# Optimization experiments

Measured on AMD Instinct MI355X. Metric: run time of the kernel, lower is better.

## Reference

```python
import jax, jax.numpy as jnp
import numpy as np
from jax import lax

BIN_NUM = 48
CPG = BIN_NUM * 3            # 144 hidden channels
NOUT = BIN_NUM + 1           # 49 symbols
K = 5                        # masked conv kernel size
H, W = 256, 512
TABLE_TOTAL = 65536.0        # EntropyTable total frequency
SCALE = 2.0 / (BIN_NUM - 1.0)


def _causal_mask(include_center: bool) -> jnp.ndarray:
    # Raster-scan causal 5x5 mask: all rows above center, left of center in
    # center row; center tap only for 'hidden' (mask-B) layers.
    m = np.zeros((K, K), np.float32)
    c = K // 2
    m[:c, :] = 1.0
    m[c, :c] = 1.0
    if include_center:
        m[c, c] = 1.0
    return jnp.asarray(m)[None, None]  # broadcast over (O, I, kh, kw)


def _mconv(x, w, b, mask):
    # x: (N, C, H, W); w: (O, I, K, K)
    y = lax.conv_general_dilated(
        x, w * mask, window_strides=(1, 1), padding='SAME',
        dimension_numbers=('NCHW', 'OIHW', 'NCHW'))
    return y + b[None, :, None, None]


def setup_inputs() -> dict:
    key = jax.random.key(0)
    ks = jax.random.split(key, 8)
    # quantized code indices in [0, BIN_NUM)
    data = jax.random.randint(ks[0], (1, 1, H, W), 0, BIN_NUM).astype(jnp.float32)
    s0 = 1.0 / np.sqrt(1 * K * K)
    sr = 1.0 / np.sqrt(CPG * K * K)
    w0 = jax.random.normal(ks[1], (CPG, 1, K, K), jnp.float32) * s0
    b0 = jnp.zeros((CPG,), jnp.float32)
    # 5 residual blocks x 2 convs = 10 hidden masked convs, stacked
    wres = jax.random.normal(ks[2], (10, CPG, CPG, K, K), jnp.float32) * sr
    bres = jnp.zeros((10, CPG), jnp.float32)
    wl = jax.random.normal(ks[3], (NOUT, CPG, K, K), jnp.float32) * sr
    bl = jnp.zeros((NOUT,), jnp.float32)
    return {"data": data, "w0": w0, "b0": b0, "wres": wres, "bres": bres,
            "wl": wl, "bl": bl}


def reference(data, w0, b0, wres, bres, wl, bl):
    mask_a = _causal_mask(False)   # first layer excludes center pixel
    mask_b = _causal_mask(True)    # hidden layers include center pixel

    # Scale(-1, 2/(bin_num-1)): map codes [0, bin_num-1] -> [-1, 1]
    x = data * SCALE - 1.0
    x = jax.nn.relu(_mconv(x, w0, b0, mask_a))
    # 5 residual blocks: y = relu(conv(relu(conv(x)))) + x
    for i in range(5):
        h1 = jax.nn.relu(_mconv(x, wres[2 * i], bres[2 * i], mask_b))
        h2 = jax.nn.relu(_mconv(h1, wres[2 * i + 1], bres[2 * i + 1], mask_b))
        x = x + h2
    logits = _mconv(x, wl, bl, mask_b)          # (1, 49, H, W)

    # EntropyTable: per-pixel softmax -> cumulative frequency table (total 65536)
    probs = jax.nn.softmax(logits, axis=1)
    cdf = jnp.cumsum(probs, axis=1) * TABLE_TOTAL
    zeros = jnp.zeros((cdf.shape[0], 1) + cdf.shape[2:], cdf.dtype)
    vec = jnp.concatenate([zeros, cdf], axis=1)  # (1, 50, H, W)
    return vec
```

## Files before the change

### kernel.cpp

```cpp
#include <hip/hip_runtime.h>

#define HH 256
#define WW 512
#define CPG 144
#define NKG 18
#define WP 516
#define HPADR 258
#define XB_E ((size_t)NKG * HPADR * WP * 8)
#define NCH 59
#define KREAL 1872
#define SCALE_F (2.0f / 47.0f)

typedef __attribute__((ext_vector_type(8))) short short8;
typedef __attribute__((ext_vector_type(4))) float floatx4;

__device__ __forceinline__ unsigned short f2bf(float f) {
    unsigned u = __builtin_bit_cast(unsigned, f);
    u += 0x7FFFu + ((u >> 16) & 1u);
    return (unsigned short)(u >> 16);
}
__device__ __forceinline__ float bf2f(unsigned short h) {
    unsigned u = ((unsigned)h) << 16;
    return __builtin_bit_cast(float, u);
}
__device__ __forceinline__ void async16(const void* g, void* l) {
    __builtin_amdgcn_global_load_lds(
        (const __attribute__((address_space(1))) unsigned int*)g,
        (__attribute__((address_space(3))) unsigned int*)l, 16, 0, 0);
}
__device__ __forceinline__ void tap_decode(int t, int& kh, int& kw) {
    kh = t < 5 ? 0 : (t < 10 ? 1 : 2);
    kw = t - (t < 5 ? 0 : (t < 10 ? 5 : 10));
}

__global__ void k_zero(float* __restrict__ p, size_t n4) {
    size_t i = (size_t)blockIdx.x * blockDim.x + threadIdx.x;
    size_t stride = (size_t)gridDim.x * blockDim.x;
    float4 z = make_float4(0.f, 0.f, 0.f, 0.f);
    for (; i < n4; i += stride) ((float4*)p)[i] = z;
}

__global__ void k_pack_hidden(const float* __restrict__ wres, unsigned short* __restrict__ wpk) {
    const int total = 10 * NCH * CPG * 32;
    int i = blockIdx.x * blockDim.x + threadIdx.x;
    int stride = gridDim.x * blockDim.x;
    for (; i < total; i += stride) {
        int kk = i & 31;
        int q  = i >> 5;
        int co = q % CPG;
        int c  = (q / CPG) % NCH;
        int l  = q / (CPG * NCH);
        int K = c * 32 + kk;
        float v = 0.f;
        if (K < KREAL) {
            int t = K / CPG, ci = K - t * CPG;
            int kh, kw; tap_decode(t, kh, kw);
            v = wres[(((size_t)(l * CPG + co) * CPG + ci) * 5 + kh) * 5 + kw];
        }
        wpk[i] = f2bf(v);
    }
}
__global__ void k_pack_final(const float* __restrict__ wl, unsigned short* __restrict__ wpkF) {
    const int total = NCH * 64 * 32;
    int i = blockIdx.x * blockDim.x + threadIdx.x;
    if (i >= total) return;
    int kk = i & 31;
    int co = (i >> 5) & 63;
    int c  = i >> 11;
    int K = c * 32 + kk;
    float v = 0.f;
    if (K < KREAL && co < 49) {
        int t = K / CPG, ci = K - t * CPG;
        int kh, kw; tap_decode(t, kh, kw);
        v = wl[(((size_t)co * CPG + ci) * 5 + kh) * 5 + kw];
    }
    wpkF[i] = f2bf(v);
}
__global__ void k_pack_small(const float* __restrict__ w0, const float* __restrict__ bl,
                             float* __restrict__ w0p, float* __restrict__ blp) {
    int i = blockIdx.x * blockDim.x + threadIdx.x;
    if (i < 12 * CPG) {
        int co = i % CPG, t = i / CPG;
        int kh, kw; tap_decode(t, kh, kw);
        w0p[i] = w0[co * 25 + kh * 5 + kw];
    } else if (i < 12 * CPG + 64) {
        int k = i - 12 * CPG;
        blp[k] = k < 49 ? bl[k] : 0.f;
    }
}

__global__ __launch_bounds__(384) void k_layer0(
    const float* __restrict__ data, const float* __restrict__ w0p,
    const float* __restrict__ b0, unsigned short* __restrict__ Xb) {
    const int lane = threadIdx.x;
    const int x = blockIdx.x * 64 + lane;
    const int y = blockIdx.y;

    float xv[12];
#pragma unroll
    for (int t = 0; t < 12; t++) {
        int kh, kw; tap_decode(t, kh, kw);
        int yy = y + kh - 2, xx = x + kw - 2;
        xv[t] = (yy >= 0 && xx >= 0 && xx < WW) ? data[yy * WW + xx] * SCALE_F - 1.0f : 0.f;
    }
#pragma unroll
    for (int kgi = 0; kgi < 3; kgi++) {
        int kg = threadIdx.y * 3 + kgi;
        float a8[8];
#pragma unroll
        for (int j = 0; j < 8; j++) a8[j] = 0.f;
#pragma unroll
        for (int t = 0; t < 12; t++)
#pragma unroll
            for (int j = 0; j < 8; j++)
                a8[j] = fmaf(w0p[t * CPG + kg * 8 + j], xv[t], a8[j]);
        short8 o;
#pragma unroll
        for (int j = 0; j < 8; j++)
            o[j] = (short)f2bf(fmaxf(a8[j] + b0[kg * 8 + j], 0.f));
        *(short8*)&Xb[((size_t)(kg * HPADR + y + 2) * WP + (x + 2)) * 8] = o;
    }
}

template<bool RES>
__global__ __launch_bounds__(768, 3) void k_conv(
    const unsigned short* __restrict__ in,
    const unsigned short* __restrict__ wq,
    const float* __restrict__ bias,
    const unsigned short* __restrict__ res,
    unsigned short* __restrict__ out) {
    __shared__ __align__(16) unsigned short As[NKG][4][132][8];
    __shared__ unsigned toff[NCH][4];
    const int tid  = threadIdx.x;
    const int lane = tid & 63;
    const int wid  = tid >> 6;
    const int ng   = wid % 3;
    const int r    = (wid / 3) & 1;
    const int ph   = wid / 6;
    const int lr = lane & 15;
    const int lg = lane >> 4;

    const int fid = blockIdx.x + (int)gridDim.x * blockIdx.y;
    const int swz = (fid & 7) * 64 + (fid >> 3);
    const int x0 = (swz & 3) * 128;
    const int y0 = (swz >> 2) * 2;

    floatx4 acc[4][3];
#pragma unroll
    for (int m = 0; m < 4; m++)
#pragma unroll
        for (int n = 0; n < 3; n++) acc[m][n] = (floatx4)0.f;

    for (int i = wid; i < 144; i += 12) {
        int half = i & 1;
        int rr   = (i >> 1) & 3;
        int kg   = i >> 3;
        async16(in + ((size_t)(kg * HPADR + y0 + rr) * WP + x0 + half * 64 + lane) * 8,
                &As[kg][rr][half * 64][0]);
    }
    if (tid < 288) {
        int kg = tid >> 4;
        int rr = (tid >> 2) & 3;
        int pxl = 128 + (tid & 3);
        *(short8*)&As[kg][rr][pxl][0] =
            *(const short8*)(in + ((size_t)(kg * HPADR + y0 + rr) * WP + x0 + pxl) * 8);
    }
    if (tid < NCH * 4) {
        int c = tid >> 2, l2 = tid & 3;
        int g = c * 4 + l2;
        if (g > 233) g = 233;
        int t = (g * 57) >> 10;
        int kgp = g - t * 18;
        int kh, kw; tap_decode(t, kh, kw);
        toff[c][l2] = (unsigned)(((kgp * 4 + kh) * 132 + kw) * 16);
    }
    asm volatile("s_waitcnt vmcnt(0) lgkmcnt(0)" ::: "memory");
    __builtin_amdgcn_s_barrier();
    __builtin_amdgcn_sched_barrier(0);

    const char* abase = (const char*)&As[0][r][ph * 64 + lr][0];
    auto LDA = [&](int c, short8 (&a)[4]) {
        const unsigned short* ap = (const unsigned short*)(abase + toff[c][lg]);
#pragma unroll
        for (int m = 0; m < 4; ++m) a[m] = *(const short8*)(ap + m * 16 * 8);
    };
    auto LDB = [&](int c, short8 (&b)[3]) {
        const unsigned short* bp = wq + (size_t)c * 4608 + (ng * 48 + lr) * 32 + lg * 8;
#pragma unroll
        for (int n = 0; n < 3; ++n) b[n] = *(const short8*)(bp + n * 512);
    };
    auto CMP = [&](const short8 (&a)[4], const short8 (&b)[3]) {
#pragma unroll
        for (int m = 0; m < 4; ++m)
#pragma unroll
            for (int n = 0; n < 3; ++n)
                acc[m][n] = __builtin_amdgcn_mfma_f32_16x16x32_bf16(a[m], b[n], acc[m][n], 0, 0, 0);
    };

    short8 a0[4], b0_[3], a1[4], b1_[3];
    LDB(0, b0_); LDA(0, a0);
#pragma unroll 1
    for (int c = 0; c < 58; c += 2) {
        LDB(c + 1, b1_); LDA(c + 1, a1);
        CMP(a0, b0_);
        LDB(c + 2, b0_); LDA(c + 2, a0);
        CMP(a1, b1_);
    }
    CMP(a0, b0_);

#pragma unroll
    for (int n = 0; n < 3; ++n) {
        int co = ng * 48 + n * 16 + lr;
        float bv = bias[co];
        const size_t pb = ((size_t)((co >> 3) * HPADR + y0 + 2 + r) * WP + (x0 + 2)) * 8 + (co & 7);
#pragma unroll
        for (int m = 0; m < 4; ++m)
#pragma unroll
            for (int rr = 0; rr < 4; ++rr) {
                int px = ph * 64 + m * 16 + lg * 4 + rr;
                size_t o = pb + (size_t)px * 8;
                float v = fmaxf(acc[m][n][rr] + bv, 0.f);
                if (RES) v += bf2f(res[o]);
                out[o] = f2bf(v);
            }
    }
}

__global__ __launch_bounds__(256, 2) void k_logits(
    const unsigned short* __restrict__ in,
    const unsigned short* __restrict__ wq,
    const float* __restrict__ blp,
    float* __restrict__ logits) {
    const int lane = threadIdx.x & 63;
    const int wid  = threadIdx.x >> 6;
    const int lr = lane & 15;
    const int lg = lane >> 4;
    const int tt = blockIdx.x * 4 + wid;
    const int y  = tt >> 2;
    const int x0 = (tt & 3) * 128;

    floatx4 acc[8][4];
#pragma unroll
    for (int m = 0; m < 8; m++)
#pragma unroll
        for (int n = 0; n < 4; n++) acc[m][n] = (floatx4)0.f;

#pragma unroll 1
    for (int c = 0; c < NCH; ++c) {
        int g = c * 4 + lg;
        if (g > 233) g = 233;
        int t = (g * 57) >> 10;
        int kgp = g - t * 18;
        int kh, kw; tap_decode(t, kh, kw);
        const unsigned short* ap =
            in + ((size_t)(kgp * HPADR + y + kh) * WP + (x0 + kw + lr)) * 8;
        const unsigned short* bp =
            wq + ((size_t)c * 64 + lr) * 32 + lg * 8;
        short8 a[8], b[4];
#pragma unroll
        for (int m = 0; m < 8; ++m) a[m] = *(const short8*)(ap + m * 128);
#pragma unroll
        for (int n = 0; n < 4; ++n) b[n] = *(const short8*)(bp + n * 512);
#pragma unroll
        for (int m = 0; m < 8; ++m)
#pragma unroll
            for (int n = 0; n < 4; ++n)
                acc[m][n] = __builtin_amdgcn_mfma_f32_16x16x32_bf16(
                    a[m], b[n], acc[m][n], 0, 0, 0);
    }

#pragma unroll
    for (int n = 0; n < 4; ++n) {
        int co = n * 16 + lr;
        float bv = blp[co];
#pragma unroll
        for (int m = 0; m < 8; ++m)
#pragma unroll
            for (int rr = 0; rr < 4; ++rr) {
                int px = m * 16 + lg * 4 + rr;
                logits[((size_t)y * WW + x0 + px) * 64 + co] = acc[m][n][rr] + bv;
            }
    }
}

__global__ __launch_bounds__(256) void k_softmax(
    const float* __restrict__ lg, float* __restrict__ out) {
    const int px = blockIdx.x * 256 + threadIdx.x;
    const int y = blockIdx.y;
    const size_t p = (size_t)y * WW + px;
    const float* l = lg + p * 64;
    float v[49];
    float m = -1e30f;
#pragma unroll
    for (int k = 0; k < 49; k++) { v[k] = l[k]; m = fmaxf(m, v[k]); }
    float s = 0.f;
#pragma unroll
    for (int k = 0; k < 49; k++) {
        v[k] = exp2f((v[k] - m) * 1.44269504088896f);
        s += v[k];
    }
    const float inv = 65536.0f / s;
    out[p] = 0.f;
    float run = 0.f;
#pragma unroll
    for (int k = 0; k < 49; k++) {
        run += v[k];
        out[(size_t)(k + 1) * (HH * WW) + p] = run * inv;
    }
}

extern "C" void kernel_launch(void* const* d_in, const int* in_sizes, int n_in,
                              void* d_out, int out_size, void* d_ws, size_t ws_size,
                              hipStream_t stream) {
    (void)in_sizes; (void)n_in; (void)out_size; (void)ws_size;
    const float* data = (const float*)d_in[0];
    const float* w0   = (const float*)d_in[1];
    const float* b0   = (const float*)d_in[2];
    const float* wres = (const float*)d_in[3];
    const float* bres = (const float*)d_in[4];
    const float* wl   = (const float*)d_in[5];
    const float* bl   = (const float*)d_in[6];
    float* out = (float*)d_out;

    char* ws = (char*)d_ws;
    unsigned short* Xb   = (unsigned short*)ws;
    unsigned short* Hb   = Xb + XB_E;
    unsigned short* wpk  = Hb + XB_E;
    unsigned short* wpkF = wpk + (size_t)10 * NCH * CPG * 32;
    float* blp  = (float*)(wpkF + (size_t)NCH * 64 * 32);
    float* w0p  = blp + 64;
    float* logits = w0p + 1728;

    k_zero<<<2048, 256, 0, stream>>>((float*)ws, (2 * XB_E * 2) / 16);

    k_pack_hidden<<<2048, 256, 0, stream>>>(wres, wpk);
    k_pack_final<<<(NCH * 64 * 32 + 255) / 256, 256, 0, stream>>>(wl, wpkF);
    k_pack_small<<<7, 256, 0, stream>>>(w0, bl, w0p, blp);

    k_layer0<<<dim3(8, 256), dim3(64, 6), 0, stream>>>(data, w0p, b0, Xb);

    const size_t LSTRIDE = (size_t)NCH * CPG * 32;
    for (int i = 0; i < 5; i++) {
        k_conv<false><<<dim3(4, 128), 768, 0, stream>>>(
            Xb, wpk + (size_t)(2 * i) * LSTRIDE, bres + (2 * i) * CPG, Xb, Hb);
        k_conv<true><<<dim3(4, 128), 768, 0, stream>>>(
            Hb, wpk + (size_t)(2 * i + 1) * LSTRIDE, bres + (2 * i + 1) * CPG, Xb, Xb);
    }

    k_logits<<<256, 256, 0, stream>>>(Xb, wpkF, blp, logits);
    k_softmax<<<dim3(2, 256), 256, 0, stream>>>(logits, out);
}
```

Baseline: 977.1 us.

## Stage logits conv input in LDS and add MFMA priority hints

Rewrites the final logits convolution to stage a 2-row by 128-pixel input halo tile in shared memory and read shifted taps from LDS, instead of each wave gathering taps from global memory. The block grows to 8 waves split across output-channel halves, rows and pixel halves, with a swizzled block order and a double-buffered load/compute loop. It also wraps the MFMA bursts in both conv kernels with sched_barrier and s_setprio so compute issues at raised priority. The cost being targeted is repeated global reads of overlapping taps and unhidden load latency, in exchange for LDS footprint and lower occupancy.

```diff
diff --git a/kernel.cpp b/kernel.cpp
--- a/kernel.cpp
+++ b/kernel.cpp
@@ -190,11 +190,15 @@
         for (int n = 0; n < 3; ++n) b[n] = *(const short8*)(bp + n * 512);
     };
     auto CMP = [&](const short8 (&a)[4], const short8 (&b)[3]) {
+        __builtin_amdgcn_sched_barrier(0);
+        __builtin_amdgcn_s_setprio(1);
 #pragma unroll
         for (int m = 0; m < 4; ++m)
 #pragma unroll
             for (int n = 0; n < 3; ++n)
                 acc[m][n] = __builtin_amdgcn_mfma_f32_16x16x32_bf16(a[m], b[n], acc[m][n], 0, 0, 0);
+        __builtin_amdgcn_s_setprio(0);
+        __builtin_amdgcn_sched_barrier(0);
     };
 
     short8 a0[4], b0_[3], a1[4], b1_[3];
@@ -226,59 +230,104 @@
     }
 }
 
-__global__ __launch_bounds__(256, 2) void k_logits(
+__global__ __launch_bounds__(512, 2) void k_logits(
     const unsigned short* __restrict__ in,
     const unsigned short* __restrict__ wq,
     const float* __restrict__ blp,
     float* __restrict__ logits) {
-    const int lane = threadIdx.x & 63;
-    const int wid  = threadIdx.x >> 6;
+    __shared__ __align__(16) unsigned short As[NKG][4][132][8];
+    __shared__ unsigned toff[NCH][4];
+    const int tid  = threadIdx.x;
+    const int lane = tid & 63;
+    const int wid  = tid >> 6;
+    const int ng   = wid & 1;
+    const int r    = (wid >> 1) & 1;
+    const int ph   = wid >> 2;
     const int lr = lane & 15;
     const int lg = lane >> 4;
-    const int tt = blockIdx.x * 4 + wid;
-    const int y  = tt >> 2;
-    const int x0 = (tt & 3) * 128;
-
-    floatx4 acc[8][4];
-#pragma unroll
-    for (int m = 0; m < 8; m++)
-#pragma unroll
-        for (int n = 0; n < 4; n++) acc[m][n] = (floatx4)0.f;
-
-#pragma unroll 1
-    for (int c = 0; c < NCH; ++c) {
-        int g = c * 4 + lg;
+
+    const int fid = blockIdx.x + (int)gridDim.x * blockIdx.y;
+    const int swz = (fid & 7) * 64 + (fid >> 3);
+    const int x0 = (swz & 3) * 128;
+    const int y0 = (swz >> 2) * 2;
+
+    floatx4 acc[4][2];
+#pragma unroll
+    for (int m = 0; m < 4; m++)
+#pragma unroll
+        for (int n = 0; n < 2; n++) acc[m][n] = (floatx4)0.f;
+
+    for (int i = wid; i < 144; i += 8) {
+        int half = i & 1;
+        int rr   = (i >> 1) & 3;
+        int kg   = i >> 3;
+        async16(in + ((size_t)(kg * HPADR + y0 + rr) * WP + x0 + half * 64 + lane) * 8,
+                &As[kg][rr][half * 64][0]);
+    }
+    if (tid < 288) {
+        int kg = tid >> 4;
+        int rr = (tid >> 2) & 3;
+        int pxl = 128 + (tid & 3);
+        *(short8*)&As[kg][rr][pxl][0] =
+            *(const short8*)(in + ((size_t)(kg * HPADR + y0 + rr) * WP + x0 + pxl) * 8);
+    }
+    if (tid < NCH * 4) {
+        int c = tid >> 2, l2 = tid & 3;
+        int g = c * 4 + l2;
         if (g > 233) g = 233;
         int t = (g * 57) >> 10;
         int kgp = g - t * 18;
         int kh, kw; tap_decode(t, kh, kw);
-        const unsigned short* ap =
-            in + ((size_t)(kgp * HPADR + y + kh) * WP + (x0 + kw + lr)) * 8;
-        const unsigned short* bp =
-            wq + ((size_t)c * 64 + lr) * 32 + lg * 8;
-        short8 a[8], b[4];
-#pragma unroll
-        for (int m = 0; m < 8; ++m) a[m] = *(const short8*)(ap + m * 128);
-#pragma unroll
-        for (int n = 0; n < 4; ++n) b[n] = *(const short8*)(bp + n * 512);
-#pragma unroll
-        for (int m = 0; m < 8; ++m)
-#pragma unroll
-            for (int n = 0; n < 4; ++n)
-                acc[m][n] = __builtin_amdgcn_mfma_f32_16x16x32_bf16(
-                    a[m], b[n], acc[m][n], 0, 0, 0);
-    }
-
-#pragma unroll
-    for (int n = 0; n < 4; ++n) {
-        int co = n * 16 + lr;
+        toff[c][l2] = (unsigned)(((kgp * 4 + kh) * 132 + kw) * 16);
+    }
+    asm volatile("s_waitcnt vmcnt(0) lgkmcnt(0)" ::: "memory");
+    __builtin_amdgcn_s_barrier();
+    __builtin_amdgcn_sched_barrier(0);
+
+    const char* abase = (const char*)&As[0][r][ph * 64 + lr][0];
+    auto LDA = [&](int c, short8 (&a)[4]) {
+        const unsigned short* ap = (const unsigned short*)(abase + toff[c][lg]);
+#pragma unroll
+        for (int m = 0; m < 4; ++m) a[m] = *(const short8*)(ap + m * 16 * 8);
+    };
+    auto LDB = [&](int c, short8 (&b)[2]) {
+        const unsigned short* bp = wq + (size_t)c * 2048 + (ng * 32 + lr) * 32 + lg * 8;
+#pragma unroll
+        for (int n = 0; n < 2; ++n) b[n] = *(const short8*)(bp + n * 512);
+    };
+    auto CMP = [&](const short8 (&a)[4], const short8 (&b)[2]) {
+        __builtin_amdgcn_sched_barrier(0);
+        __builtin_amdgcn_s_setprio(1);
+#pragma unroll
+        for (int m = 0; m < 4; ++m)
+#pragma unroll
+            for (int n = 0; n < 2; ++n)
+                acc[m][n] = __builtin_amdgcn_mfma_f32_16x16x32_bf16(a[m], b[n], acc[m][n], 0, 0, 0);
+        __builtin_amdgcn_s_setprio(0);
+        __builtin_amdgcn_sched_barrier(0);
+    };
+
+    short8 a0[4], b0_[2], a1[4], b1_[2];
+    LDB(0, b0_); LDA(0, a0);
+#pragma unroll 1
+    for (int c = 0; c < 58; c += 2) {
+        LDB(c + 1, b1_); LDA(c + 1, a1);
+        CMP(a0, b0_);
+        LDB(c + 2, b0_); LDA(c + 2, a0);
+        CMP(a1, b1_);
+    }
+    CMP(a0, b0_);
+
+#pragma unroll
+    for (int n = 0; n < 2; ++n) {
+        int co = ng * 32 + n * 16 + lr;
         float bv = blp[co];
 #pragma unroll
-        for (int m = 0; m < 8; ++m)
+        for (int m = 0; m < 4; ++m)
 #pragma unroll
             for (int rr = 0; rr < 4; ++rr) {
-                int px = m * 16 + lg * 4 + rr;
-                logits[((size_t)y * WW + x0 + px) * 64 + co] = acc[m][n][rr] + bv;
+                int px = ph * 64 + m * 16 + lg * 4 + rr;
+                logits[((size_t)(y0 + r) * WW + x0 + px) * 64 + co] = acc[m][n][rr] + bv;
             }
     }
 }
@@ -347,6 +396,6 @@
             Hb, wpk + (size_t)(2 * i + 1) * LSTRIDE, bres + (2 * i + 1) * CPG, Xb, Xb);
     }
 
-    k_logits<<<256, 256, 0, stream>>>(Xb, wpkF, blp, logits);
+    k_logits<<<dim3(4, 128), 512, 0, stream>>>(Xb, wpkF, blp, logits);
     k_softmax<<<dim3(2, 256), 256, 0, stream>>>(logits, out);
 }
```

Result: faster. 911.3 us (-6.7%).
